# Kernel tuning notes

Hardware: AMD Instinct MI355X
Metric: run time of the kernel (lower is better)

Reference implementation:

```python
import jax, jax.numpy as jnp
import numpy as np

N_NODES = 10000
N_EDGES = 160000
N_FEAT = 512
HEADS = 8
HID = 128
OUT = 16


def setup_inputs() -> dict:
    key = jax.random.key(0)
    ks = jax.random.split(key, 16)
    inp = {
        'node_features': jax.random.normal(ks[0], (N_NODES, N_FEAT), jnp.float32),
        'edge_src': jax.random.randint(ks[1], (N_EDGES,), 0, N_NODES, jnp.int32),
        'edge_dst': jax.random.randint(ks[2], (N_EDGES,), 0, N_NODES, jnp.int32),
        # GAT layer params (scaled randn for numerical sanity)
        'W1': jax.random.normal(ks[3], (HEADS, HID, N_FEAT), jnp.float32) * 0.05,
        'a1': jax.random.normal(ks[4], (HEADS, 2 * HID), jnp.float32) * 0.05,
        'W2': jax.random.normal(ks[5], (HEADS, HID, HID), jnp.float32) * 0.05,
        'a2': jax.random.normal(ks[6], (HEADS, 2 * HID), jnp.float32) * 0.05,
        # MLP: LayerNorm(128) -> Linear(128,64) -> LeakyReLU -> Linear(64,16) -> LeakyReLU -> Linear(16,OUT) -> ReLU
        'ln_g': jnp.ones((HID,), jnp.float32),
        'ln_b': jnp.zeros((HID,), jnp.float32),
        'Wl1': jax.random.normal(ks[7], (64, HID), jnp.float32) * 0.05,
        'bl1': jnp.zeros((64,), jnp.float32),
        'Wl2': jax.random.normal(ks[8], (16, 64), jnp.float32) * 0.05,
        'bl2': jnp.zeros((16,), jnp.float32),
        'Wl3': jax.random.normal(ks[9], (OUT, 16), jnp.float32) * 0.05,
        'bl3': jnp.zeros((OUT,), jnp.float32),
    }
    return inp


def gat_layer(x, src, dst, W, a, n_nodes):
    # per-node, per-head projection: h[n,h,d]
    h = jnp.einsum('hdf,nf->nhd', W, x)
    # split attention vector: e_ij = a[:HID].h_i + a[HID:].h_j
    s_i = jnp.einsum('nhd,hd->nh', h, a[:, :HID])  # score contribution of target i
    s_j = jnp.einsum('nhd,hd->nh', h, a[:, HID:])  # score contribution of neighbor j
    e = jax.nn.leaky_relu(s_i[dst] + s_j[src])     # [E,H], negative_slope=0.01 (torch default)
    # segment softmax over edges grouped by dst
    m = jax.ops.segment_max(e, dst, num_segments=n_nodes)           # [N,H]
    m = jnp.where(jnp.isfinite(m), m, 0.0)
    ex = jnp.exp(e - m[dst])                                        # [E,H]
    denom = jax.ops.segment_sum(ex, dst, num_segments=n_nodes)      # [N,H]
    alpha = ex / jnp.where(denom > 0, denom, 1.0)[dst]              # [E,H]
    # scatter-accumulate weighted neighbor embeddings
    agg = jax.ops.segment_sum(alpha[:, :, None] * h[src], dst, num_segments=n_nodes)  # [N,H,HID]
    # average over heads, ELU (matches 1/attn_heads * attn_sum -> ELU)
    return jax.nn.elu(agg.mean(axis=1))  # [N,HID]


def reference(node_features, edge_src, edge_dst, W1, a1, W2, a2,
              ln_g, ln_b, Wl1, bl1, Wl2, bl2, Wl3, bl3):
    n = node_features.shape[0]
    emb1 = gat_layer(node_features, edge_src, edge_dst, W1, a1, n)
    emb2 = gat_layer(emb1, edge_src, edge_dst, W2, a2, n)
    g = emb2.mean(axis=0)  # [HID] graph embedding
    # MLP head (dropout = identity at inference)
    mu = g.mean()
    var = ((g - mu) ** 2).mean()
    gn = (g - mu) / jnp.sqrt(var + 1e-5) * ln_g + ln_b
    x = jax.nn.leaky_relu(Wl1 @ gn + bl1)
    x = jax.nn.leaky_relu(Wl2 @ x + bl2)
    return jax.nn.relu(Wl3 @ x + bl3)
```

## Files before the change

kernel.cpp:

```cpp
#include <hip/hip_runtime.h>
#include <math.h>

#define N_NODES 10000
#define N_EDGES 160000
#define N_FEAT  512
#define HEADS   8
#define HID     128

typedef __attribute__((ext_vector_type(8))) short bf16x8;
typedef __attribute__((ext_vector_type(4))) float f32x4;
typedef __attribute__((ext_vector_type(2))) float v2f;

__device__ inline unsigned short f2bf_rne(float f) {
  unsigned int u = __float_as_uint(f);
  unsigned int r = u + 0x7fffu + ((u >> 16) & 1u);
  return (unsigned short)(r >> 16);
}
__device__ inline float bf2f(unsigned int b) {
  return __uint_as_float(b << 16);
}

__device__ inline void split_body(const float* __restrict__ in,
                                  unsigned short* __restrict__ hi,
                                  unsigned short* __restrict__ lo,
                                  int R, int K8, int idx) {
  int r = idx & 15;
  int t = idx >> 4;
  int kq = t % K8;
  int rb = t / K8;
  int row = rb * 16 + r;
  float v[8] = {0.f, 0.f, 0.f, 0.f, 0.f, 0.f, 0.f, 0.f};
  if (row < R) {
    const float* p = in + (size_t)row * (K8 * 8) + kq * 8;
    float4 a = *(const float4*)p;
    float4 b = *(const float4*)(p + 4);
    v[0] = a.x; v[1] = a.y; v[2] = a.z; v[3] = a.w;
    v[4] = b.x; v[5] = b.y; v[6] = b.z; v[7] = b.w;
  }
  union { unsigned short u[8]; int4 v4; } H, L;
  #pragma unroll
  for (int e = 0; e < 8; ++e) {
    unsigned short hb_ = f2bf_rne(v[e]);
    H.u[e] = hb_;
    L.u[e] = f2bf_rne(v[e] - bf2f(hb_));
  }
  *(int4*)&hi[(size_t)idx * 8] = H.v4;
  *(int4*)&lo[(size_t)idx * 8] = L.v4;
}

__global__ __launch_bounds__(256)
void split_frag2(const float* __restrict__ in1, unsigned short* __restrict__ hi1,
                 unsigned short* __restrict__ lo1, int R1, int K81, int total1,
                 int nb1,
                 const float* __restrict__ in2, unsigned short* __restrict__ hi2,
                 unsigned short* __restrict__ lo2, int R2, int K82, int total2,
                 int nb2,
                 const int* __restrict__ edst, int* __restrict__ deg, int E) {
  if ((int)blockIdx.x < nb1) {
    int idx = blockIdx.x * 256 + threadIdx.x;
    if (idx < total1) split_body(in1, hi1, lo1, R1, K81, idx);
  } else if ((int)blockIdx.x < nb1 + nb2) {
    int idx = (blockIdx.x - nb1) * 256 + threadIdx.x;
    if (idx < total2) split_body(in2, hi2, lo2, R2, K82, idx);
  } else {
    int e = (blockIdx.x - nb1 - nb2) * 256 + threadIdx.x;
    if (e < E) atomicAdd(&deg[edst[e]], 1);
  }
}

__global__ __launch_bounds__(128, 3)
void gemm_frag(const unsigned short* __restrict__ Afh,
               const unsigned short* __restrict__ Afl,
               const unsigned short* __restrict__ Bfh,
               const unsigned short* __restrict__ Bfl,
               const float* __restrict__ avec,
               unsigned short* __restrict__ hb,
               float* __restrict__ si, float* __restrict__ sj,
               int M, int K) {
  __shared__ float rsi[64][2];
  __shared__ float rsj[64][2];
  int tid = threadIdx.x;
  int wave = tid >> 6, lane = tid & 63;
  int r = lane & 15, q = lane >> 4;

  int blk = blockIdx.x;
  int rr = blk & 7, gg = blk >> 3;
  int head = gg & 7;
  int mtile = (gg >> 3) * 8 + rr;
  int m0 = mtile * 64;
  int wn = wave * 64;
  int K8 = K >> 3;

  const bf16x8* pAh = (const bf16x8*)Afh;
  const bf16x8* pAl = (const bf16x8*)Afl;
  const bf16x8* pBh = (const bf16x8*)Bfh;
  const bf16x8* pBl = (const bf16x8*)Bfl;
  size_t rstep = (size_t)K8 * 16;
  size_t aidx = (size_t)(m0 >> 4) * rstep + (size_t)q * 16 + r;
  size_t bidx = (size_t)(head * 8 + (wn >> 4)) * rstep + (size_t)q * 16 + r;

  f32x4 acc[4][4] = {};

  for (int k0 = 0; k0 < K; k0 += 32, aidx += 64, bidx += 64) {
    bf16x8 ah[4], al[4], bh[4], bl[4];
    #pragma unroll
    for (int i = 0; i < 4; ++i) {
      ah[i] = pAh[aidx + i * rstep];
      al[i] = pAl[aidx + i * rstep];
      bh[i] = pBh[bidx + i * rstep];
      bl[i] = pBl[bidx + i * rstep];
    }
    #pragma unroll
    for (int i = 0; i < 4; ++i)
      #pragma unroll
      for (int j = 0; j < 4; ++j) {
        acc[i][j] = __builtin_amdgcn_mfma_f32_16x16x32_bf16(ah[i], bh[j], acc[i][j], 0, 0, 0);
        acc[i][j] = __builtin_amdgcn_mfma_f32_16x16x32_bf16(ah[i], bl[j], acc[i][j], 0, 0, 0);
        acc[i][j] = __builtin_amdgcn_mfma_f32_16x16x32_bf16(al[i], bh[j], acc[i][j], 0, 0, 0);
      }
  }

  const float* av = avec + (size_t)head * (2 * HID);
  float aiv[4], ajv[4];
  #pragma unroll
  for (int j = 0; j < 4; ++j) {
    int c = wn + j * 16 + r;
    aiv[j] = av[c];
    ajv[j] = av[HID + c];
  }
  #pragma unroll
  for (int i = 0; i < 4; ++i) {
    #pragma unroll
    for (int reg = 0; reg < 4; ++reg) {
      int lrow = i * 16 + q * 4 + reg;
      int row = m0 + lrow;
      float vsi = 0.f, vsj = 0.f;
      #pragma unroll
      for (int j = 0; j < 4; ++j) {
        float v = acc[i][j][reg];
        vsi = fmaf(v, aiv[j], vsi);
        vsj = fmaf(v, ajv[j], vsj);
        if (row < M)
          hb[((size_t)head * M + row) * HID + wn + j * 16 + r] = f2bf_rne(v);
      }
      #pragma unroll
      for (int o = 8; o >= 1; o >>= 1) {
        vsi += __shfl_xor(vsi, o);
        vsj += __shfl_xor(vsj, o);
      }
      if (r == 0) {
        rsi[lrow][wave] = vsi;
        rsj[lrow][wave] = vsj;
      }
    }
  }
  __syncthreads();
  if (tid < 64) {
    int row = m0 + tid;
    if (row < M) {
      si[(size_t)head * M + row] = rsi[tid][0] + rsi[tid][1];
      sj[(size_t)head * M + row] = rsj[tid][0] + rsj[tid][1];
    }
  }
}

__global__ __launch_bounds__(1024)
void scan_kernel(const int* __restrict__ deg, int* __restrict__ off, int N) {
  __shared__ int sums[1024];
  const int PER = 10;
  int tid = threadIdx.x;
  int base = tid * PER;
  int loc[PER];
  int run = 0;
  #pragma unroll
  for (int j = 0; j < PER; ++j) {
    int v = (base + j < N) ? deg[base + j] : 0;
    run += v;
    loc[j] = run;
  }
  sums[tid] = run;
  __syncthreads();
  for (int o = 1; o < 1024; o <<= 1) {
    int v = (tid >= o) ? sums[tid - o] : 0;
    __syncthreads();
    sums[tid] += v;
    __syncthreads();
  }
  int ex = sums[tid] - run;
  if (tid == 0) off[0] = 0;
  #pragma unroll
  for (int j = 0; j < PER; ++j)
    if (base + j < N) off[base + j + 1] = ex + loc[j];
}

__global__ void fill_kernel(const int* __restrict__ src, const int* __restrict__ dst,
                            const int* __restrict__ off, int* __restrict__ cursor,
                            int* __restrict__ ssrc, int E) {
  int e = blockIdx.x * blockDim.x + threadIdx.x;
  if (e < E) {
    int d = dst[e];
    int p = atomicAdd(&cursor[d], 1);
    ssrc[off[d] + p] = src[e];
  }
}

__global__ __launch_bounds__(512)
void gat_aggregate7(const unsigned short* __restrict__ hb,
                    const float* __restrict__ si, const float* __restrict__ sj,
                    const int* __restrict__ off, const int* __restrict__ ssrc,
                    unsigned short* __restrict__ aggb, int N) {
  __shared__ int2 prs[8][64];
  int head = blockIdx.x & 7;
  int wv = threadIdx.x >> 6;
  int n = (blockIdx.x >> 3) * 8 + wv;
  int lane = threadIdx.x & 63;
  int grp = lane >> 4;
  int l = lane & 15;
  const unsigned short* hbase = hb + (size_t)head * N * HID;
  const float* sjh = sj + (size_t)head * N;
  int begin = off[n], end = off[n + 1];
  int deg = end - begin;
  int dmin = deg < 64 ? deg : 64;
  float s_i = si[(size_t)head * N + n];

  int src0 = 0;
  float sc0 = -INFINITY;
  if (lane < deg) {
    src0 = ssrc[begin + lane];
    float t = s_i + sjh[src0];
    sc0 = t > 0.f ? t : 0.01f * t;
  }
  float m = sc0;
  for (int e2 = 64 + lane; e2 < deg; e2 += 64) {
    int s = ssrc[begin + e2];
    float t = s_i + sjh[s];
    t = t > 0.f ? t : 0.01f * t;
    m = fmaxf(m, t);
  }
  #pragma unroll
  for (int o = 1; o <= 32; o <<= 1) m = fmaxf(m, __shfl_xor(m, o));

  float w0 = (lane < deg) ? __expf(sc0 - m) : 0.f;
  float den = w0;
  for (int e2 = 64 + lane; e2 < deg; e2 += 64) {
    int s = ssrc[begin + e2];
    float t = s_i + sjh[s];
    t = t > 0.f ? t : 0.01f * t;
    den += __expf(t - m);
  }
  #pragma unroll
  for (int o = 1; o <= 32; o <<= 1) den += __shfl_xor(den, o);

  prs[wv][lane] = make_int2(src0, __float_as_int(w0));
  __asm__ volatile("s_waitcnt lgkmcnt(0)" ::: "memory");

  v2f a01 = {0.f, 0.f}, a23 = {0.f, 0.f}, a45 = {0.f, 0.f}, a67 = {0.f, 0.f};

  for (int e0 = 0; e0 < dmin; e0 += 16) {
    float we[4];
    int se[4];
    #pragma unroll
    for (int u = 0; u < 4; ++u) {
      int e = e0 + u * 4 + grp;
      int2 p = prs[wv][e];
      se[u] = p.x;
      we[u] = __int_as_float(p.y);
    }
    int4 pv[4];
    #pragma unroll
    for (int u = 0; u < 4; ++u)
      pv[u] = *(const int4*)&hbase[(size_t)se[u] * HID + l * 8];
    #pragma unroll
    for (int u = 0; u < 4; ++u) {
      v2f w2 = {we[u], we[u]};
      int4 p = pv[u];
      v2f t0 = {bf2f((unsigned)p.x & 0xffffu), __uint_as_float((unsigned)p.x & 0xffff0000u)};
      v2f t1 = {bf2f((unsigned)p.y & 0xffffu), __uint_as_float((unsigned)p.y & 0xffff0000u)};
      v2f t2 = {bf2f((unsigned)p.z & 0xffffu), __uint_as_float((unsigned)p.z & 0xffff0000u)};
      v2f t3 = {bf2f((unsigned)p.w & 0xffffu), __uint_as_float((unsigned)p.w & 0xffff0000u)};
      a01 += w2 * t0;
      a23 += w2 * t1;
      a45 += w2 * t2;
      a67 += w2 * t3;
    }
  }
  for (int e2 = 64; e2 < deg; e2 += 4) {
    int e = e2 + grp;
    bool valid = e < deg;
    int s = ssrc[valid ? begin + e : begin];
    float t = s_i + sjh[s];
    t = t > 0.f ? t : 0.01f * t;
    float wu = valid ? __expf(t - m) : 0.f;
    v2f w2 = {wu, wu};
    int4 p = *(const int4*)&hbase[(size_t)s * HID + l * 8];
    v2f t0 = {bf2f((unsigned)p.x & 0xffffu), __uint_as_float((unsigned)p.x & 0xffff0000u)};
    v2f t1 = {bf2f((unsigned)p.y & 0xffffu), __uint_as_float((unsigned)p.y & 0xffff0000u)};
    v2f t2 = {bf2f((unsigned)p.z & 0xffffu), __uint_as_float((unsigned)p.z & 0xffff0000u)};
    v2f t3 = {bf2f((unsigned)p.w & 0xffffu), __uint_as_float((unsigned)p.w & 0xffff0000u)};
    a01 += w2 * t0; a23 += w2 * t1; a45 += w2 * t2; a67 += w2 * t3;
  }

  #pragma unroll
  for (int o = 16; o <= 32; o <<= 1) {
    a01.x += __shfl_xor(a01.x, o); a01.y += __shfl_xor(a01.y, o);
    a23.x += __shfl_xor(a23.x, o); a23.y += __shfl_xor(a23.y, o);
    a45.x += __shfl_xor(a45.x, o); a45.y += __shfl_xor(a45.y, o);
    a67.x += __shfl_xor(a67.x, o); a67.y += __shfl_xor(a67.y, o);
  }

  if (grp == 0) {
    float inv = den > 0.f ? 1.0f / den : 0.f;
    union { unsigned short u[8]; int4 v4; } P;
    P.u[0] = f2bf_rne(a01.x * inv); P.u[1] = f2bf_rne(a01.y * inv);
    P.u[2] = f2bf_rne(a23.x * inv); P.u[3] = f2bf_rne(a23.y * inv);
    P.u[4] = f2bf_rne(a45.x * inv); P.u[5] = f2bf_rne(a45.y * inv);
    P.u[6] = f2bf_rne(a67.x * inv); P.u[7] = f2bf_rne(a67.y * inv);
    *(int4*)&aggb[((size_t)head * N + n) * HID + l * 8] = P.v4;
  }
}

__global__ __launch_bounds__(256)
void headmean_frag_w2(const unsigned short* __restrict__ aggb,
                      unsigned short* __restrict__ hiA, unsigned short* __restrict__ loA,
                      int N, int nbHM,
                      const float* __restrict__ W2, unsigned short* __restrict__ hiB,
                      unsigned short* __restrict__ loB, int totalB) {
  if ((int)blockIdx.x >= nbHM) {
    int idx = (blockIdx.x - nbHM) * 256 + threadIdx.x;
    if (idx < totalB) split_body(W2, hiB, loB, HEADS * HID, 16, idx);
    return;
  }
  int idx = blockIdx.x * 256 + threadIdx.x;
  int total = ((N + 15) / 16) * 256;
  if (idx >= total) return;
  int r = idx & 15;
  int kq = (idx >> 4) & 15;
  int rb = idx >> 8;
  int n = rb * 16 + r;
  float s[8] = {0.f, 0.f, 0.f, 0.f, 0.f, 0.f, 0.f, 0.f};
  if (n < N) {
    #pragma unroll
    for (int hh = 0; hh < HEADS; ++hh) {
      int4 pv = *(const int4*)&aggb[((size_t)hh * N + n) * HID + kq * 8];
      s[0] += bf2f((unsigned)pv.x & 0xffffu);
      s[1] += __uint_as_float((unsigned)pv.x & 0xffff0000u);
      s[2] += bf2f((unsigned)pv.y & 0xffffu);
      s[3] += __uint_as_float((unsigned)pv.y & 0xffff0000u);
      s[4] += bf2f((unsigned)pv.z & 0xffffu);
      s[5] += __uint_as_float((unsigned)pv.z & 0xffff0000u);
      s[6] += bf2f((unsigned)pv.w & 0xffffu);
      s[7] += __uint_as_float((unsigned)pv.w & 0xffff0000u);
    }
  }
  union { unsigned short u[8]; int4 v4; } H, L;
  #pragma unroll
  for (int e = 0; e < 8; ++e) {
    float v = s[e] * (1.0f / HEADS);
    v = v > 0.f ? v : (__expf(v) - 1.0f);
    unsigned short hb_ = f2bf_rne(v);
    H.u[e] = hb_;
    L.u[e] = f2bf_rne(v - bf2f(hb_));
  }
  *(int4*)&hiA[(size_t)idx * 8] = H.v4;
  *(int4*)&loA[(size_t)idx * 8] = L.v4;
}

__global__ __launch_bounds__(256)
void headmean_pool(const unsigned short* __restrict__ aggb, float* __restrict__ g,
                   int N) {
  __shared__ float sm[16][128];
  int t = threadIdx.x;
  int nl = t >> 4, dg = t & 15;
  int n = blockIdx.x * 16 + nl;
  float v[8] = {0.f, 0.f, 0.f, 0.f, 0.f, 0.f, 0.f, 0.f};
  if (n < N) {
    #pragma unroll
    for (int hh = 0; hh < HEADS; ++hh) {
      int4 pv = *(const int4*)&aggb[((size_t)hh * N + n) * HID + dg * 8];
      v[0] += bf2f((unsigned)pv.x & 0xffffu);
      v[1] += __uint_as_float((unsigned)pv.x & 0xffff0000u);
      v[2] += bf2f((unsigned)pv.y & 0xffffu);
      v[3] += __uint_as_float((unsigned)pv.y & 0xffff0000u);
      v[4] += bf2f((unsigned)pv.z & 0xffffu);
      v[5] += __uint_as_float((unsigned)pv.z & 0xffff0000u);
      v[6] += bf2f((unsigned)pv.w & 0xffffu);
      v[7] += __uint_as_float((unsigned)pv.w & 0xffff0000u);
    }
    #pragma unroll
    for (int e = 0; e < 8; ++e) {
      float x = v[e] * (1.0f / HEADS);
      v[e] = x > 0.f ? x : (__expf(x) - 1.0f);
    }
  }
  #pragma unroll
  for (int e = 0; e < 8; ++e) sm[nl][dg * 8 + e] = v[e];
  __syncthreads();
  if (t < 128) {
    float s = 0.f;
    #pragma unroll
    for (int nn = 0; nn < 16; ++nn) s += sm[nn][t];
    atomicAdd(&g[t], s);
  }
}

__global__ __launch_bounds__(128)
void mlp_kernel(const float* __restrict__ g, const float* __restrict__ ln_g,
                const float* __restrict__ ln_b, const float* __restrict__ Wl1,
                const float* __restrict__ bl1, const float* __restrict__ Wl2,
                const float* __restrict__ bl2, const float* __restrict__ Wl3,
                const float* __restrict__ bl3, float* __restrict__ out, float invN) {
  __shared__ float red[128];
  __shared__ float gn[128];
  __shared__ float x1[64];
  __shared__ float x2[16];
  int t = threadIdx.x;
  float gg = g[t] * invN;
  red[t] = gg;
  __syncthreads();
  for (int o = 64; o > 0; o >>= 1) {
    if (t < o) red[t] += red[t + o];
    __syncthreads();
  }
  float mu = red[0] * (1.0f / HID);
  __syncthreads();
  float dv = gg - mu;
  red[t] = dv * dv;
  __syncthreads();
  for (int o = 64; o > 0; o >>= 1) {
    if (t < o) red[t] += red[t + o];
    __syncthreads();
  }
  float var = red[0] * (1.0f / HID);
  gn[t] = dv / sqrtf(var + 1e-5f) * ln_g[t] + ln_b[t];
  __syncthreads();
  if (t < 64) {
    float s = bl1[t];
    for (int k = 0; k < 128; ++k) s += Wl1[t * 128 + k] * gn[k];
    x1[t] = s > 0.f ? s : 0.01f * s;
  }
  __syncthreads();
  if (t < 16) {
    float s = bl2[t];
    for (int k = 0; k < 64; ++k) s += Wl2[t * 64 + k] * x1[k];
    x2[t] = s > 0.f ? s : 0.01f * s;
  }
  __syncthreads();
  if (t < 16) {
    float s = bl3[t];
    for (int k = 0; k < 16; ++k) s += Wl3[t * 16 + k] * x2[k];
    out[t] = s > 0.f ? s : 0.f;
  }
}

extern "C" void kernel_launch(void* const* d_in, const int* in_sizes, int n_in,
                              void* d_out, int out_size, void* d_ws, size_t ws_size,
                              hipStream_t stream) {
  const float* x    = (const float*)d_in[0];
  const int*   esrc = (const int*)d_in[1];
  const int*   edst = (const int*)d_in[2];
  const float* W1   = (const float*)d_in[3];
  const float* a1   = (const float*)d_in[4];
  const float* W2   = (const float*)d_in[5];
  const float* a2   = (const float*)d_in[6];
  const float* ln_g = (const float*)d_in[7];
  const float* ln_b = (const float*)d_in[8];
  const float* Wl1  = (const float*)d_in[9];
  const float* bl1  = (const float*)d_in[10];
  const float* Wl2  = (const float*)d_in[11];
  const float* bl2  = (const float*)d_in[12];
  const float* Wl3  = (const float*)d_in[13];
  const float* bl3  = (const float*)d_in[14];
  float* out = (float*)d_out;

  const int RBPAD = 640;

  unsigned short* aggb = (unsigned short*)d_ws;
  float* si   = (float*)(aggb + (size_t)N_NODES * HEADS * HID);
  float* sj   = si + N_NODES * HEADS;
  float* g    = sj + N_NODES * HEADS;
  int*   deg  = (int*)(g + 128);
  int*   cur  = deg + N_NODES;
  int*   off  = cur + N_NODES;
  int*   ssrc = off + 10004;
  unsigned short* Afh = (unsigned short*)(ssrc + N_EDGES);
  unsigned short* Afl = Afh + (size_t)RBPAD * 64 * 128;
  unsigned short* Bfh = Afl + (size_t)RBPAD * 64 * 128;
  unsigned short* Bfl = Bfh + (size_t)64 * 64 * 128;
  unsigned short* hb  = Bfl + (size_t)64 * 64 * 128;

  hipMemsetAsync(g, 0, 128 * sizeof(float) + 2 * N_NODES * sizeof(int), stream);

  int gemmGrid = 160 * HEADS;
  int aggGrid = (N_NODES / 8) * 8;

  {
    int totalA = RBPAD * 64 * 16;
    int nbA = (totalA + 255) / 256;
    int totalB = 64 * 64 * 16;
    int nbB = (totalB + 255) / 256;
    int nbE = (N_EDGES + 255) / 256;
    split_frag2<<<nbA + nbB + nbE, 256, 0, stream>>>(
        x, Afh, Afl, N_NODES, 64, totalA, nbA,
        W1, Bfh, Bfl, HEADS * HID, 64, totalB, nbB,
        edst, deg, N_EDGES);
  }
  scan_kernel<<<1, 1024, 0, stream>>>(deg, off, N_NODES);
  fill_kernel<<<(N_EDGES + 255) / 256, 256, 0, stream>>>(esrc, edst, off, cur, ssrc, N_EDGES);

  gemm_frag<<<gemmGrid, 128, 0, stream>>>(Afh, Afl, Bfh, Bfl, a1, hb,
                                          si, sj, N_NODES, N_FEAT);
  gat_aggregate7<<<aggGrid, 512, 0, stream>>>(hb, si, sj, off, ssrc, aggb, N_NODES);
  {
    int nbHM = ((N_NODES + 15) / 16 * 256 + 255) / 256;
    int totalB = 64 * 16 * 16;
    int nbB = (totalB + 255) / 256;
    headmean_frag_w2<<<nbHM + nbB, 256, 0, stream>>>(aggb, Afh, Afl, N_NODES, nbHM,
                                                     W2, Bfh, Bfl, totalB);
  }

  gemm_frag<<<gemmGrid, 128, 0, stream>>>(Afh, Afl, Bfh, Bfl, a2, hb,
                                          si, sj, N_NODES, HID);
  gat_aggregate7<<<aggGrid, 512, 0, stream>>>(hb, si, sj, off, ssrc, aggb, N_NODES);

  headmean_pool<<<(N_NODES + 15) / 16, 256, 0, stream>>>(aggb, g, N_NODES);
  mlp_kernel<<<1, 128, 0, stream>>>(g, ln_g, ln_b, Wl1, bl1, Wl2, bl2, Wl3, bl3,
                                    out, 1.0f / N_NODES);
}
```

Before: 299.9 us.

## Map one node per 16-lane group in GAT aggregation instead of per wavefront

The aggregation kernel now assigns each destination node to a 16-lane subgroup, so a wavefront handles four nodes at once rather than one. With an average degree of about 16, the old one-wave-per-node mapping left most lanes idle during the score and softmax phases and needed cross-group shuffle reductions. Reductions now span only 16 lanes, and the final cross-group accumulator reduction is removed. The trade-off is divergence between the four nodes in a wave whose degrees differ, and nodes above 32 edges fall back to a serial per-edge loop.

```diff
diff --git a/kernel.cpp b/kernel.cpp
--- a/kernel.cpp
+++ b/kernel.cpp
@@ -205,117 +205,113 @@
 }
 
 __global__ __launch_bounds__(512)
-void gat_aggregate7(const unsigned short* __restrict__ hb,
+void gat_aggregate8(const unsigned short* __restrict__ hb,
                     const float* __restrict__ si, const float* __restrict__ sj,
                     const int* __restrict__ off, const int* __restrict__ ssrc,
                     unsigned short* __restrict__ aggb, int N) {
-  __shared__ int2 prs[8][64];
+  __shared__ int2 prs[8][4][32];
   int head = blockIdx.x & 7;
   int wv = threadIdx.x >> 6;
-  int n = (blockIdx.x >> 3) * 8 + wv;
   int lane = threadIdx.x & 63;
   int grp = lane >> 4;
-  int l = lane & 15;
+  int sl = lane & 15;
+  int n = (blockIdx.x >> 3) * 32 + wv * 4 + grp;
   const unsigned short* hbase = hb + (size_t)head * N * HID;
   const float* sjh = sj + (size_t)head * N;
-  int begin = off[n], end = off[n + 1];
-  int deg = end - begin;
-  int dmin = deg < 64 ? deg : 64;
-  float s_i = si[(size_t)head * N + n];
-
-  int src0 = 0;
-  float sc0 = -INFINITY;
-  if (lane < deg) {
-    src0 = ssrc[begin + lane];
+  bool nv = n < N;
+  int begin = 0, deg = 0;
+  float s_i = 0.f;
+  if (nv) {
+    begin = off[n];
+    deg = off[n + 1] - begin;
+    s_i = si[(size_t)head * N + n];
+  }
+
+  int src0 = 0, src1 = 0;
+  float sc0 = -INFINITY, sc1 = -INFINITY;
+  if (sl < deg) {
+    src0 = ssrc[begin + sl];
     float t = s_i + sjh[src0];
     sc0 = t > 0.f ? t : 0.01f * t;
   }
-  float m = sc0;
-  for (int e2 = 64 + lane; e2 < deg; e2 += 64) {
+  if (16 + sl < deg) {
+    src1 = ssrc[begin + 16 + sl];
+    float t = s_i + sjh[src1];
+    sc1 = t > 0.f ? t : 0.01f * t;
+  }
+  float m = fmaxf(sc0, sc1);
+  for (int e2 = 32 + sl; e2 < deg; e2 += 16) {
     int s = ssrc[begin + e2];
     float t = s_i + sjh[s];
     t = t > 0.f ? t : 0.01f * t;
     m = fmaxf(m, t);
   }
   #pragma unroll
-  for (int o = 1; o <= 32; o <<= 1) m = fmaxf(m, __shfl_xor(m, o));
-
-  float w0 = (lane < deg) ? __expf(sc0 - m) : 0.f;
-  float den = w0;
-  for (int e2 = 64 + lane; e2 < deg; e2 += 64) {
+  for (int o = 1; o <= 8; o <<= 1) m = fmaxf(m, __shfl_xor(m, o));
+
+  float w0 = (sl < deg) ? __expf(sc0 - m) : 0.f;
+  float w1 = (16 + sl < deg) ? __expf(sc1 - m) : 0.f;
+  float den = w0 + w1;
+  for (int e2 = 32 + sl; e2 < deg; e2 += 16) {
     int s = ssrc[begin + e2];
     float t = s_i + sjh[s];
     t = t > 0.f ? t : 0.01f * t;
     den += __expf(t - m);
   }
   #pragma unroll
-  for (int o = 1; o <= 32; o <<= 1) den += __shfl_xor(den, o);
-
-  prs[wv][lane] = make_int2(src0, __float_as_int(w0));
+  for (int o = 1; o <= 8; o <<= 1) den += __shfl_xor(den, o);
+
+  prs[wv][grp][sl] = make_int2(src0, __float_as_int(w0));
+  prs[wv][grp][16 + sl] = make_int2(src1, __float_as_int(w1));
   __asm__ volatile("s_waitcnt lgkmcnt(0)" ::: "memory");
 
   v2f a01 = {0.f, 0.f}, a23 = {0.f, 0.f}, a45 = {0.f, 0.f}, a67 = {0.f, 0.f};
-
-  for (int e0 = 0; e0 < dmin; e0 += 16) {
-    float we[4];
-    int se[4];
+  int dmin = deg < 32 ? deg : 32;
+  for (int e0 = 0; e0 < dmin; e0 += 4) {
+    int2 p[4];
+    #pragma unroll
+    for (int u = 0; u < 4; ++u) p[u] = prs[wv][grp][e0 + u];
+    int4 pv[4];
+    #pragma unroll
+    for (int u = 0; u < 4; ++u)
+      pv[u] = *(const int4*)&hbase[(size_t)p[u].x * HID + sl * 8];
     #pragma unroll
     for (int u = 0; u < 4; ++u) {
-      int e = e0 + u * 4 + grp;
-      int2 p = prs[wv][e];
-      se[u] = p.x;
-      we[u] = __int_as_float(p.y);
-    }
-    int4 pv[4];
-    #pragma unroll
-    for (int u = 0; u < 4; ++u)
-      pv[u] = *(const int4*)&hbase[(size_t)se[u] * HID + l * 8];
-    #pragma unroll
-    for (int u = 0; u < 4; ++u) {
-      v2f w2 = {we[u], we[u]};
-      int4 p = pv[u];
-      v2f t0 = {bf2f((unsigned)p.x & 0xffffu), __uint_as_float((unsigned)p.x & 0xffff0000u)};
-      v2f t1 = {bf2f((unsigned)p.y & 0xffffu), __uint_as_float((unsigned)p.y & 0xffff0000u)};
-      v2f t2 = {bf2f((unsigned)p.z & 0xffffu), __uint_as_float((unsigned)p.z & 0xffff0000u)};
-      v2f t3 = {bf2f((unsigned)p.w & 0xffffu), __uint_as_float((unsigned)p.w & 0xffff0000u)};
+      float w = __int_as_float(p[u].y);
+      v2f w2 = {w, w};
+      int4 q = pv[u];
+      v2f t0 = {bf2f((unsigned)q.x & 0xffffu), __uint_as_float((unsigned)q.x & 0xffff0000u)};
+      v2f t1 = {bf2f((unsigned)q.y & 0xffffu), __uint_as_float((unsigned)q.y & 0xffff0000u)};
+      v2f t2 = {bf2f((unsigned)q.z & 0xffffu), __uint_as_float((unsigned)q.z & 0xffff0000u)};
+      v2f t3 = {bf2f((unsigned)q.w & 0xffffu), __uint_as_float((unsigned)q.w & 0xffff0000u)};
       a01 += w2 * t0;
       a23 += w2 * t1;
       a45 += w2 * t2;
       a67 += w2 * t3;
     }
   }
-  for (int e2 = 64; e2 < deg; e2 += 4) {
-    int e = e2 + grp;
-    bool valid = e < deg;
-    int s = ssrc[valid ? begin + e : begin];
+  for (int e2 = 32; e2 < deg; ++e2) {
+    int s = ssrc[begin + e2];
     float t = s_i + sjh[s];
     t = t > 0.f ? t : 0.01f * t;
-    float wu = valid ? __expf(t - m) : 0.f;
-    v2f w2 = {wu, wu};
-    int4 p = *(const int4*)&hbase[(size_t)s * HID + l * 8];
-    v2f t0 = {bf2f((unsigned)p.x & 0xffffu), __uint_as_float((unsigned)p.x & 0xffff0000u)};
-    v2f t1 = {bf2f((unsigned)p.y & 0xffffu), __uint_as_float((unsigned)p.y & 0xffff0000u)};
-    v2f t2 = {bf2f((unsigned)p.z & 0xffffu), __uint_as_float((unsigned)p.z & 0xffff0000u)};
-    v2f t3 = {bf2f((unsigned)p.w & 0xffffu), __uint_as_float((unsigned)p.w & 0xffff0000u)};
+    float w = __expf(t - m);
+    v2f w2 = {w, w};
+    int4 q = *(const int4*)&hbase[(size_t)s * HID + sl * 8];
+    v2f t0 = {bf2f((unsigned)q.x & 0xffffu), __uint_as_float((unsigned)q.x & 0xffff0000u)};
+    v2f t1 = {bf2f((unsigned)q.y & 0xffffu), __uint_as_float((unsigned)q.y & 0xffff0000u)};
+    v2f t2 = {bf2f((unsigned)q.z & 0xffffu), __uint_as_float((unsigned)q.z & 0xffff0000u)};
+    v2f t3 = {bf2f((unsigned)q.w & 0xffffu), __uint_as_float((unsigned)q.w & 0xffff0000u)};
     a01 += w2 * t0; a23 += w2 * t1; a45 += w2 * t2; a67 += w2 * t3;
   }
 
-  #pragma unroll
-  for (int o = 16; o <= 32; o <<= 1) {
-    a01.x += __shfl_xor(a01.x, o); a01.y += __shfl_xor(a01.y, o);
-    a23.x += __shfl_xor(a23.x, o); a23.y += __shfl_xor(a23.y, o);
-    a45.x += __shfl_xor(a45.x, o); a45.y += __shfl_xor(a45.y, o);
-    a67.x += __shfl_xor(a67.x, o); a67.y += __shfl_xor(a67.y, o);
-  }
-
-  if (grp == 0) {
+  if (nv) {
     float inv = den > 0.f ? 1.0f / den : 0.f;
     union { unsigned short u[8]; int4 v4; } P;
     P.u[0] = f2bf_rne(a01.x * inv); P.u[1] = f2bf_rne(a01.y * inv);
     P.u[2] = f2bf_rne(a23.x * inv); P.u[3] = f2bf_rne(a23.y * inv);
     P.u[4] = f2bf_rne(a45.x * inv); P.u[5] = f2bf_rne(a45.y * inv);
     P.u[6] = f2bf_rne(a67.x * inv); P.u[7] = f2bf_rne(a67.y * inv);
-    *(int4*)&aggb[((size_t)head * N + n) * HID + l * 8] = P.v4;
+    *(int4*)&aggb[((size_t)head * N + n) * HID + sl * 8] = P.v4;
   }
 }
 
@@ -491,7 +487,7 @@
   hipMemsetAsync(g, 0, 128 * sizeof(float) + 2 * N_NODES * sizeof(int), stream);
 
   int gemmGrid = 160 * HEADS;
-  int aggGrid = (N_NODES / 8) * 8;
+  int aggGrid = ((N_NODES + 31) / 32) * 8;
 
   {
     int totalA = RBPAD * 64 * 16;
@@ -509,7 +505,7 @@
 
   gemm_frag<<<gemmGrid, 128, 0, stream>>>(Afh, Afl, Bfh, Bfl, a1, hb,
                                           si, sj, N_NODES, N_FEAT);
-  gat_aggregate7<<<aggGrid, 512, 0, stream>>>(hb, si, sj, off, ssrc, aggb, N_NODES);
+  gat_aggregate8<<<aggGrid, 512, 0, stream>>>(hb, si, sj, off, ssrc, aggb, N_NODES);
   {
     int nbHM = ((N_NODES + 15) / 16 * 256 + 255) / 256;
     int totalB = 64 * 16 * 16;
@@ -520,7 +516,7 @@
 
   gemm_frag<<<gemmGrid, 128, 0, stream>>>(Afh, Afl, Bfh, Bfl, a2, hb,
                                           si, sj, N_NODES, HID);
-  gat_aggregate7<<<aggGrid, 512, 0, stream>>>(hb, si, sj, off, ssrc, aggb, N_NODES);
+  gat_aggregate8<<<aggGrid, 512, 0, stream>>>(hb, si, sj, off, ssrc, aggb, N_NODES);
 
   headmean_pool<<<(N_NODES + 15) / 16, 256, 0, stream>>>(aggb, g, N_NODES);
   mlp_kernel<<<1, 128, 0, stream>>>(g, ln_g, ln_b, Wl1, bl1, Wl2, bl2, Wl3, bl3,
```

Result: faster. 263.7 us (-12.1%).
